# Performance work log

Measured on AMD Instinct MI355X. Metric: run time of the kernel, lower is better.

The kernel has to match this reference:

```python
import jax, jax.numpy as jnp
import numpy as np
import math

B, S, H = 2, 2048, 2048
NH, NKV, HD = 16, 4, 128


def _rope_tables(seq_len, head_dim):
    # Standard RoPE: freqs over half dim, duplicated to full head_dim.
    inv_freq = 1.0 / (10000.0 ** (np.arange(0, head_dim, 2, dtype=np.float32) / head_dim))
    t = np.arange(seq_len, dtype=np.float32)
    freqs = np.outer(t, inv_freq)  # [S, HD/2]
    emb = np.concatenate([freqs, freqs], axis=-1)  # [S, HD]
    return jnp.asarray(np.cos(emb)), jnp.asarray(np.sin(emb))


def setup_inputs() -> dict:
    key = jax.random.key(0)
    k1, k2, k3, k4 = jax.random.split(key, 4)
    cos, sin = _rope_tables(S, HD)
    return {
        "x": jax.random.normal(k1, (B, S, H), dtype=jnp.float32),
        "cos": cos,
        "sin": sin,
        "Wq": jax.random.normal(k2, (H, NH * HD), dtype=jnp.float32) * (1.0 / math.sqrt(H)),
        "Wkv": jax.random.normal(k3, (H, 2 * NKV * HD), dtype=jnp.float32) * (1.0 / math.sqrt(H)),
        "Wo": jax.random.normal(k4, (NH * HD, H), dtype=jnp.float32) * (1.0 / math.sqrt(NH * HD)),
    }


def _rotate_half(x):
    x1, x2 = jnp.split(x, 2, axis=-1)
    return jnp.concatenate([-x2, x1], axis=-1)


def _apply_rotary(x, cos, sin):
    # x: [B, S, nheads, HD]; cos/sin: [S, HD]
    c = cos[None, :, None, :]
    s = sin[None, :, None, :]
    return x * c + _rotate_half(x) * s


def reference(x, cos, sin, Wq, Wkv, Wo):
    b, s, _ = x.shape
    q = (x @ Wq).reshape(b, s, NH, HD)
    kv = x @ Wkv
    k, v = jnp.split(kv, [NKV * HD], axis=-1)
    k = k.reshape(b, s, NKV, HD)
    v = v.reshape(b, s, NKV, HD)
    q = _apply_rotary(q, cos, sin)
    k = _apply_rotary(k, cos, sin)
    # to [B, heads, S, HD]
    q = jnp.transpose(q, (0, 2, 1, 3))
    k = jnp.transpose(k, (0, 2, 1, 3))
    v = jnp.transpose(v, (0, 2, 1, 3))
    # GQA: repeat K/V heads
    rep = NH // NKV
    k = jnp.repeat(k, rep, axis=1)
    v = jnp.repeat(v, rep, axis=1)
    scale = jnp.asarray(1.0 / math.sqrt(HD), dtype=x.dtype)
    scores = jnp.einsum('bhqd,bhkd->bhqk', q * scale, k)  # [B, NH, S, S]
    causal = jnp.tril(jnp.ones((s, s), dtype=jnp.bool_))
    scores = jnp.where(causal, scores, jnp.asarray(-jnp.inf, scores.dtype))
    attn = jax.nn.softmax(scores, axis=-1)
    out = jnp.einsum('bhqk,bhkd->bhqd', attn, v)
    out = jnp.transpose(out, (0, 2, 1, 3)).reshape(b, s, NH * HD)
    return out @ Wo
```

## Files before the change

kernel.cpp:

```cpp
#include <hip/hip_runtime.h>
#include <math.h>

#define NB 2
#define SEQ 2048
#define HDIM 2048
#define NHD 16
#define NKVH 4
#define HEADD 128
#define MROWS (NB*SEQ)
#define NQCOLS (NHD*HEADD)
#define QKVCOLS 3072

typedef unsigned short ushortT;
typedef __attribute__((ext_vector_type(8))) short short8;
typedef __attribute__((ext_vector_type(4))) float floatx4;
typedef __attribute__((ext_vector_type(4))) unsigned short ushort4v;

__device__ __forceinline__ ushortT f2bf(float f) {
  union { float f; unsigned int u; } v; v.f = f;
  unsigned int r = v.u + 0x7FFFu + ((v.u >> 16) & 1u);
  return (ushortT)(r >> 16);
}
__device__ __forceinline__ float bf2f(ushortT u) {
  union { unsigned int u; float f; } v; v.u = ((unsigned int)u) << 16;
  return v.f;
}

__device__ __forceinline__ unsigned int cvt_pk_bf16(float lo, float hi) {
  unsigned int r;
  asm("v_cvt_pk_bf16_f32 %0, %1, %2" : "=v"(r) : "v"(lo), "v"(hi));
  return r;
}

__device__ __forceinline__ void gload16(const ushortT* g, ushortT* l) {
  __builtin_amdgcn_global_load_lds(
      (const __attribute__((address_space(1))) void*)g,
      (__attribute__((address_space(3))) void*)l, 16, 0, 0);
}

__device__ __forceinline__ void tile_barrier() {
  asm volatile("" ::: "memory");
  __builtin_amdgcn_s_barrier();
  asm volatile("" ::: "memory");
  __builtin_amdgcn_sched_barrier(0);
}

__global__ __launch_bounds__(256) void cast_bf16_kernel(
    const float* __restrict__ in, ushortT* __restrict__ out, int n4) {
  int i = blockIdx.x * 256 + threadIdx.x;
  if (i >= n4) return;
  float4 v = ((const float4*)in)[i];
  ushort4v o;
  o.x = f2bf(v.x); o.y = f2bf(v.y); o.z = f2bf(v.z); o.w = f2bf(v.w);
  ((ushort4v*)out)[i] = o;
}

__global__ __launch_bounds__(256) void transpose_cast3_kernel(
    const float* __restrict__ Wq, const float* __restrict__ Wkv,
    const float* __restrict__ Wo, ushortT* __restrict__ out) {
  __shared__ ushortT tile[32][33];
  int cu0 = blockIdx.x * 32, r0 = blockIdx.y * 32;
  const float* src; int C, c0;
  if (cu0 < 2048)      { src = Wq;  C = 2048; c0 = cu0; }
  else if (cu0 < 3072) { src = Wkv; C = 1024; c0 = cu0 - 2048; }
  else                 { src = Wo;  C = 2048; c0 = cu0 - 3072; }
  int tx = threadIdx.x & 31, ty = threadIdx.x >> 5;
#pragma unroll
  for (int i = 0; i < 4; ++i)
    tile[ty + i*8][tx] = f2bf(src[(size_t)(r0 + ty + i*8) * C + c0 + tx]);
  __syncthreads();
#pragma unroll
  for (int i = 0; i < 4; ++i)
    out[(size_t)(cu0 + ty + i*8) * 2048 + r0 + tx] = tile[tx][ty + i*8];
}

template <int MH>
__global__ __launch_bounds__(512, 2) void gemm_ring_kernel(
    const ushortT* __restrict__ A, const ushortT* __restrict__ Bt,
    void* __restrict__ C, int M, int N, int K, int c_fp32) {
  constexpr int BM = 128 * MH;
  __shared__ __align__(16) ushortT lA[4][BM * 32];
  __shared__ __align__(16) ushortT lB[4][256 * 32];
  const int m0 = blockIdx.y * BM;
  const int n0 = blockIdx.x * 256;
  const int tid = threadIdx.x;
  const int lane = tid & 63, wave = tid >> 6;
  const int g = lane >> 4, l15 = lane & 15;
  const int wr = wave >> 2, wc = wave & 3;
  const int wm = wr * (BM / 2), wn = wc * 64;

  floatx4 acc[4 * MH][4] = {};

  auto stageA = [&](int u) {
    ushortT* dst = lA[u & 3];
    const int kt = u << 5;
#pragma unroll
    for (int i = 0; i < MH; ++i) {
      int s = i * 512 + tid;
      int r = s >> 2, j = s & 3;
      int jj = j ^ ((r >> 1) & 3);
      gload16(A + (size_t)(m0 + r) * K + kt + jj * 8, dst + s * 8);
    }
  };
  auto stageB = [&](int u) {
    ushortT* dst = lB[u & 3];
    const int kt = u << 5;
#pragma unroll
    for (int i = 0; i < 2; ++i) {
      int s = i * 512 + tid;
      int r = s >> 2, j = s & 3;
      int jj = j ^ ((r >> 1) & 3);
      gload16(Bt + (size_t)(n0 + r) * K + kt + jj * 8, dst + s * 8);
    }
  };

  stageA(0); stageB(0); stageA(1); stageB(1); stageA(2); stageB(2);

  const int NT = K >> 5;
  for (int u = 0; u < NT; ++u) {
    if constexpr (MH == 2) {
      if (u + 2 < NT)      asm volatile("s_waitcnt vmcnt(8)" ::: "memory");
      else if (u + 1 < NT) asm volatile("s_waitcnt vmcnt(4)" ::: "memory");
      else                 asm volatile("s_waitcnt vmcnt(0)" ::: "memory");
    } else {
      if (u + 2 < NT)      asm volatile("s_waitcnt vmcnt(6)" ::: "memory");
      else if (u + 1 < NT) asm volatile("s_waitcnt vmcnt(3)" ::: "memory");
      else                 asm volatile("s_waitcnt vmcnt(0)" ::: "memory");
    }
    tile_barrier();

    const ushortT* la = lA[u & 3];
    const ushortT* lb = lB[u & 3];
    const bool more = (u + 3) < NT;

    short8 bfr[4];
#pragma unroll
    for (int nt = 0; nt < 4; ++nt) {
      int col = wn + nt * 16 + l15;
      bfr[nt] = *(const short8*)(lb + col * 32 + (g ^ ((col >> 1) & 3)) * 8);
    }

#pragma unroll
    for (int mh = 0; mh < MH; ++mh) {
      if (mh) tile_barrier();
      short8 afr[4];
#pragma unroll
      for (int mt = 0; mt < 4; ++mt) {
        int row = wm + mh * 64 + mt * 16 + l15;
        afr[mt] = *(const short8*)(la + row * 32 + (g ^ ((row >> 1) & 3)) * 8);
      }
      if (more) {
        if (mh == 0) stageA(u + 3);
        if (mh == MH - 1) stageB(u + 3);
      }
      __builtin_amdgcn_s_setprio(1);
#pragma unroll
      for (int mt = 0; mt < 4; ++mt)
#pragma unroll
        for (int nt = 0; nt < 4; ++nt)
          acc[mh * 4 + mt][nt] = __builtin_amdgcn_mfma_f32_16x16x32_bf16(
              afr[mt], bfr[nt], acc[mh * 4 + mt][nt], 0, 0, 0);
      __builtin_amdgcn_s_setprio(0);
    }
  }

#pragma unroll
  for (int fm = 0; fm < 4 * MH; ++fm)
#pragma unroll
    for (int nt = 0; nt < 4; ++nt)
#pragma unroll
      for (int r4 = 0; r4 < 4; ++r4) {
        int row = m0 + wm + fm * 16 + g * 4 + r4;
        int col = n0 + wn + nt * 16 + l15;
        float v = acc[fm][nt][r4];
        if (c_fp32) ((float*)C)[(size_t)row * N + col] = v;
        else ((ushortT*)C)[(size_t)row * N + col] = f2bf(v);
      }
}

__global__ __launch_bounds__(256) void rope_qk_kernel(
    const ushortT* __restrict__ QKVtmp, const float* __restrict__ cosT,
    const float* __restrict__ sinT, ushortT* __restrict__ Qr,
    ushortT* __restrict__ Kr) {
  int idx = blockIdx.x * 256 + threadIdx.x;
  if (idx < NB * SEQ * NHD * 64) {
    int d = idx & 63;
    int t = idx >> 6;
    int h = t & (NHD - 1);
    int bs = t >> 4;
    int s = bs & (SEQ - 1);
    int b = bs >> 11;
    float c = cosT[s * HEADD + d], sn = sinT[s * HEADD + d];
    float q1 = bf2f(QKVtmp[(size_t)bs * QKVCOLS + h * HEADD + d]);
    float q2 = bf2f(QKVtmp[(size_t)bs * QKVCOLS + h * HEADD + d + 64]);
    size_t o = ((size_t)(b * NHD + h) * SEQ + s) * HEADD + d;
    Qr[o]      = f2bf(q1 * c - q2 * sn);
    Qr[o + 64] = f2bf(q2 * c + q1 * sn);
  } else {
    int k = idx - NB * SEQ * NHD * 64;
    int d = k & 63;
    int t = k >> 6;
    int kvh = t & (NKVH - 1);
    int bs = t >> 2;
    int s = bs & (SEQ - 1);
    int b = bs >> 11;
    float c = cosT[s * HEADD + d], sn = sinT[s * HEADD + d];
    float k1 = bf2f(QKVtmp[(size_t)bs * QKVCOLS + 2048 + kvh * HEADD + d]);
    float k2 = bf2f(QKVtmp[(size_t)bs * QKVCOLS + 2048 + kvh * HEADD + d + 64]);
    size_t o = ((size_t)(b * NKVH + kvh) * SEQ + s) * HEADD + d;
    Kr[o]      = f2bf(k1 * c - k2 * sn);
    Kr[o + 64] = f2bf(k2 * c + k1 * sn);
  }
}

__global__ __launch_bounds__(256) void v_relayout_kernel(
    const ushortT* __restrict__ QKVtmp, ushortT* __restrict__ Vt) {
  __shared__ ushortT tile[32][33];
  int bk = blockIdx.z;
  int b = bk >> 2, kvh = bk & 3;
  int s0 = blockIdx.x * 32, d0 = blockIdx.y * 32;
  int tx = threadIdx.x & 31, ty = threadIdx.x >> 5;
#pragma unroll
  for (int i = 0; i < 4; ++i) {
    int s = s0 + ty + i * 8;
    tile[ty + i * 8][tx] =
        QKVtmp[(size_t)(b * SEQ + s) * QKVCOLS + 2560 + kvh * HEADD + d0 + tx];
  }
  __syncthreads();
#pragma unroll
  for (int i = 0; i < 4; ++i) {
    int d = d0 + ty + i * 8;
    Vt[((size_t)bk * HEADD + d) * SEQ + s0 + tx] = tile[tx][ty + i * 8];
  }
}

__global__ __launch_bounds__(256, 2) void attn_kernel(
    const ushortT* __restrict__ Q,
    const ushortT* __restrict__ Kg,
    const ushortT* __restrict__ Vg,
    ushortT* __restrict__ Oa) {
  __shared__ __align__(16) ushortT lK[2][64 * 128];
  __shared__ __align__(16) ushortT lV[2][128 * 64];
  __shared__ __align__(16) ushortT lP[4 * 32 * 64];

  const int tid = threadIdx.x;
  const int w = tid >> 6, lane = tid & 63;
  const int g = lane >> 4, l15 = lane & 15;
  const int sw = l15 & 7;
  const int bh = blockIdx.x;
  const int b = bh >> 4, h = bh & 15;
  const int kvh = h >> 2;
  const int yi = blockIdx.y;
  const int qi = (yi < 8) ? (15 - yi) : (yi - 8);
  const int q0 = qi << 7;
  const int qw = q0 + w * 32;
  const int nkt = 2 * qi + 2;

  const float SC = 0.08838834764831845f * 1.4426950408889634f;
  const float THR = 8.0f / SC;

  const ushortT* kbase = Kg + ((size_t)(b * NKVH + kvh)) * SEQ * HEADD;
  const ushortT* vbase = Vg + ((size_t)(b * NKVH + kvh)) * HEADD * SEQ;
  ushortT* pw = lP + w * 32 * 64;

  short8 qf[2][4];
#pragma unroll
  for (int mt = 0; mt < 2; ++mt) {
    const ushortT* qp =
        Q + (((size_t)(b * NHD + h)) * SEQ + qw + mt * 16 + l15) * HEADD + g * 8;
#pragma unroll
    for (int ks = 0; ks < 4; ++ks) qf[mt][ks] = *(const short8*)(qp + ks * 32);
  }

  floatx4 o[2][8] = {};
  float m_s[2] = {-INFINITY, -INFINITY};
  float l_s[2] = {0.f, 0.f};

  auto stage = [&](int kt, int buf) {
#pragma unroll
    for (int ii = 0; ii < 4; ++ii) {
      int s = ii * 256 + tid;
      int r = s >> 4, j = (s & 15) ^ (r & 7);
      gload16(kbase + (size_t)(kt * 64 + r) * HEADD + j * 8, lK[buf] + s * 8);
    }
#pragma unroll
    for (int ii = 0; ii < 4; ++ii) {
      int s = ii * 256 + tid;
      int r = s >> 3, j = (s & 7) ^ (r & 7);
      gload16(vbase + (size_t)r * SEQ + kt * 64 + j * 8, lV[buf] + s * 8);
    }
  };

  stage(0, 0);
  asm volatile("s_waitcnt vmcnt(0)" ::: "memory");
  __builtin_amdgcn_s_barrier();

  for (int kt = 0; kt < nkt; ++kt) {
    const int cur = kt & 1;
    if (kt + 1 < nkt) stage(kt + 1, cur ^ 1);

    const int kb = kt * 64;
    const int rel0 = qw - kb;
    const int rel1 = qw + 16 - kb;

    floatx4 sc[2][4] = {};
    __builtin_amdgcn_s_setprio(1);
#pragma unroll
    for (int nt = 0; nt < 4; ++nt) {
      if (nt * 16 > rel1 + 15) continue;
      const bool need0 = (nt * 16 <= rel0 + 15);
#pragma unroll
      for (int ks = 0; ks < 4; ++ks) {
        short8 kf = *(const short8*)(lK[cur] + (nt * 16 + l15) * 128 + ((ks * 4 + g) ^ sw) * 8);
        sc[1][nt] = __builtin_amdgcn_mfma_f32_16x16x32_bf16(kf, qf[1][ks], sc[1][nt], 0, 0, 0);
        if (need0)
          sc[0][nt] = __builtin_amdgcn_mfma_f32_16x16x32_bf16(kf, qf[0][ks], sc[0][nt], 0, 0, 0);
      }
    }
    __builtin_amdgcn_s_setprio(0);

#pragma unroll
    for (int mt = 0; mt < 2; ++mt) {
      const int qsub = qw + mt * 16;
      if (kb > qsub + 15) continue;
      const bool needmask = (kb + 63) > qsub;
      float ps[4][4];
      float mx = -INFINITY;
#pragma unroll
      for (int nt = 0; nt < 4; ++nt)
#pragma unroll
        for (int r = 0; r < 4; ++r) {
          float v = sc[mt][nt][r];
          if (needmask) {
            int kg = kb + nt * 16 + g * 4 + r;
            if (kg > qsub + l15) v = -INFINITY;
          }
          ps[nt][r] = v;
          mx = fmaxf(mx, v);
        }
      mx = fmaxf(mx, __shfl_xor(mx, 16));
      mx = fmaxf(mx, __shfl_xor(mx, 32));

      float mn;
      if (__all(mx <= m_s[mt] + THR)) {
        mn = m_s[mt];
      } else {
        mn = fmaxf(m_s[mt], mx);
        float alpha = __builtin_amdgcn_exp2f((m_s[mt] - mn) * SC);
        l_s[mt] *= alpha;
#pragma unroll
        for (int dt = 0; dt < 8; ++dt)
#pragma unroll
          for (int r = 0; r < 4; ++r) o[mt][dt][r] *= alpha;
        m_s[mt] = mn;
      }
      const float mnSC = mn * SC;

      float rs = 0.f;
#pragma unroll
      for (int nt = 0; nt < 4; ++nt) {
        float e[4];
#pragma unroll
        for (int r = 0; r < 4; ++r) {
          e[r] = __builtin_amdgcn_exp2f(__builtin_fmaf(ps[nt][r], SC, -mnSC));
          rs += e[r];
        }
        uint2 pk;
        pk.x = cvt_pk_bf16(e[0], e[1]);
        pk.y = cvt_pk_bf16(e[2], e[3]);
        *(uint2*)(pw + (mt * 16 + l15) * 64 +
                  (((nt * 2 + (g >> 1)) ^ sw) * 8 + (g & 1) * 4)) = pk;
      }
      rs += __shfl_xor(rs, 16);
      rs += __shfl_xor(rs, 32);
      l_s[mt] += rs;
    }

    __builtin_amdgcn_s_setprio(1);
#pragma unroll
    for (int ks = 0; ks < 2; ++ks) {
      const bool n1 = (kb + ks * 32 <= qw + 31);
      if (!n1) continue;
      const bool n0 = (kb + ks * 32 <= qw + 15);
      short8 bp1 = *(const short8*)(pw + (16 + l15) * 64 + ((ks * 4 + g) ^ sw) * 8);
      short8 bp0;
      if (n0) bp0 = *(const short8*)(pw + l15 * 64 + ((ks * 4 + g) ^ sw) * 8);
#pragma unroll
      for (int dt = 0; dt < 8; ++dt) {
        short8 vf = *(const short8*)(lV[cur] + (dt * 16 + l15) * 64 + ((ks * 4 + g) ^ sw) * 8);
        o[1][dt] = __builtin_amdgcn_mfma_f32_16x16x32_bf16(vf, bp1, o[1][dt], 0, 0, 0);
        if (n0)
          o[0][dt] = __builtin_amdgcn_mfma_f32_16x16x32_bf16(vf, bp0, o[0][dt], 0, 0, 0);
      }
    }
    __builtin_amdgcn_s_setprio(0);

    asm volatile("s_waitcnt vmcnt(0)" ::: "memory");
    __builtin_amdgcn_s_barrier();
  }

#pragma unroll
  for (int mt = 0; mt < 2; ++mt) {
    float inv = 1.f / l_s[mt];
    int qg = qw + mt * 16 + l15;
#pragma unroll
    for (int dt = 0; dt < 8; ++dt) {
      uint2 ov;
      ov.x = cvt_pk_bf16(o[mt][dt][0] * inv, o[mt][dt][1] * inv);
      ov.y = cvt_pk_bf16(o[mt][dt][2] * inv, o[mt][dt][3] * inv);
      *(uint2*)(Oa + (size_t)(b * SEQ + qg) * NQCOLS + h * HEADD + dt * 16 + g * 4) = ov;
    }
  }
}

extern "C" void kernel_launch(void* const* d_in, const int* in_sizes, int n_in,
                              void* d_out, int out_size, void* d_ws, size_t ws_size,
                              hipStream_t stream) {
  const float* x    = (const float*)d_in[0];
  const float* cosT = (const float*)d_in[1];
  const float* sinT = (const float*)d_in[2];
  const float* Wq   = (const float*)d_in[3];
  const float* Wkv  = (const float*)d_in[4];
  const float* Wo   = (const float*)d_in[5];

  char* ws = (char*)d_ws;
  ushortT* x_bf   = (ushortT*)(ws + 0);
  ushortT* Wqkvt  = (ushortT*)(ws + 16777216);
  ushortT* Wot    = (ushortT*)(ws + 29360128);
  ushortT* QKVtmp = (ushortT*)(ws + 37748736);
  ushortT* Qr     = (ushortT*)(ws + 62914560);
  ushortT* Kr     = (ushortT*)(ws + 79691776);
  ushortT* Vt     = (ushortT*)(ws + 83886080);
  ushortT* Oattn  = QKVtmp;

  cast_bf16_kernel<<<8192, 256, 0, stream>>>(x, x_bf, (MROWS * HDIM) / 4);
  transpose_cast3_kernel<<<dim3(160, 64), 256, 0, stream>>>(Wq, Wkv, Wo, Wqkvt);

  gemm_ring_kernel<2><<<dim3(12, 16), 512, 0, stream>>>(x_bf, Wqkvt, QKVtmp,
                                                        MROWS, QKVCOLS, HDIM, 0);

  rope_qk_kernel<<<20480, 256, 0, stream>>>(QKVtmp, cosT, sinT, Qr, Kr);
  v_relayout_kernel<<<dim3(64, 4, 8), 256, 0, stream>>>(QKVtmp, Vt);

  attn_kernel<<<dim3(32, 16), 256, 0, stream>>>(Qr, Kr, Vt, Oattn);

  gemm_ring_kernel<1><<<dim3(8, 32), 512, 0, stream>>>(Oattn, Wot, d_out,
                                                       MROWS, HDIM, NQCOLS, 1);
}
```

Measured before the change: 344.0 us.

## Pair causal query tiles per block with triple-buffered K/V pipeline

Each attention block now processes two query tiles (a long one and its short complement), so every block does the same amount of causal work, and the grid is halved. The K/V staging moves from double to triple buffering with partial vmcnt waits, letting loads run two tiles ahead and continue across the boundary between the two query tiles. Occupancy drops to one block per CU and LDS use rises, so latency hiding now relies on the deeper pipeline rather than a second resident block.

```diff
diff --git a/kernel.cpp b/kernel.cpp
--- a/kernel.cpp
+++ b/kernel.cpp
@@ -234,13 +234,13 @@
   }
 }
 
-__global__ __launch_bounds__(256, 2) void attn_kernel(
+__global__ __launch_bounds__(256, 1) void attn_kernel(
     const ushortT* __restrict__ Q,
     const ushortT* __restrict__ Kg,
     const ushortT* __restrict__ Vg,
     ushortT* __restrict__ Oa) {
-  __shared__ __align__(16) ushortT lK[2][64 * 128];
-  __shared__ __align__(16) ushortT lV[2][128 * 64];
+  __shared__ __align__(16) ushortT lK[3][64 * 128];
+  __shared__ __align__(16) ushortT lV[3][128 * 64];
   __shared__ __align__(16) ushortT lP[4 * 32 * 64];
 
   const int tid = threadIdx.x;
@@ -251,10 +251,10 @@
   const int b = bh >> 4, h = bh & 15;
   const int kvh = h >> 2;
   const int yi = blockIdx.y;
-  const int qi = (yi < 8) ? (15 - yi) : (yi - 8);
-  const int q0 = qi << 7;
-  const int qw = q0 + w * 32;
-  const int nkt = 2 * qi + 2;
+  const int qiA = 15 - yi;
+  const int qiB = yi;
+  const int nA = 2 * qiA + 2, nB = 2 * qiB + 2;
+  const int ntot = nA + nB;
 
   const float SC = 0.08838834764831845f * 1.4426950408889634f;
   const float THR = 8.0f / SC;
@@ -263,13 +263,21 @@
   const ushortT* vbase = Vg + ((size_t)(b * NKVH + kvh)) * HEADD * SEQ;
   ushortT* pw = lP + w * 32 * 64;
 
-  short8 qf[2][4];
+  const int qwA = (qiA << 7) + w * 32;
+  const int qwB = (qiB << 7) + w * 32;
+
+  short8 qfA[2][4], qfB[2][4];
 #pragma unroll
   for (int mt = 0; mt < 2; ++mt) {
-    const ushortT* qp =
-        Q + (((size_t)(b * NHD + h)) * SEQ + qw + mt * 16 + l15) * HEADD + g * 8;
-#pragma unroll
-    for (int ks = 0; ks < 4; ++ks) qf[mt][ks] = *(const short8*)(qp + ks * 32);
+    const ushortT* qpA =
+        Q + (((size_t)(b * NHD + h)) * SEQ + qwA + mt * 16 + l15) * HEADD + g * 8;
+    const ushortT* qpB =
+        Q + (((size_t)(b * NHD + h)) * SEQ + qwB + mt * 16 + l15) * HEADD + g * 8;
+#pragma unroll
+    for (int ks = 0; ks < 4; ++ks) {
+      qfA[mt][ks] = *(const short8*)(qpA + ks * 32);
+      qfB[mt][ks] = *(const short8*)(qpB + ks * 32);
+    }
   }
 
   floatx4 o[2][8] = {};
@@ -290,15 +298,11 @@
       gload16(vbase + (size_t)r * SEQ + kt * 64 + j * 8, lV[buf] + s * 8);
     }
   };
-
-  stage(0, 0);
-  asm volatile("s_waitcnt vmcnt(0)" ::: "memory");
-  __builtin_amdgcn_s_barrier();
-
-  for (int kt = 0; kt < nkt; ++kt) {
-    const int cur = kt & 1;
-    if (kt + 1 < nkt) stage(kt + 1, cur ^ 1);
-
+  auto stage_job = [&](int jj) {
+    if (jj < ntot) stage(jj < nA ? jj : jj - nA, jj % 3);
+  };
+
+  auto compute = [&](const short8 (&qf)[2][4], int qw, int kt, int cur) {
     const int kb = kt * 64;
     const int rel0 = qw - kb;
     const int rel1 = qw + 16 - kb;
@@ -394,23 +398,49 @@
       }
     }
     __builtin_amdgcn_s_setprio(0);
-
-    asm volatile("s_waitcnt vmcnt(0)" ::: "memory");
-    __builtin_amdgcn_s_barrier();
-  }
-
+  };
+
+  auto epilogue = [&](int qw) {
+#pragma unroll
+    for (int mt = 0; mt < 2; ++mt) {
+      float inv = 1.f / l_s[mt];
+      int qg = qw + mt * 16 + l15;
+#pragma unroll
+      for (int dt = 0; dt < 8; ++dt) {
+        uint2 ov;
+        ov.x = cvt_pk_bf16(o[mt][dt][0] * inv, o[mt][dt][1] * inv);
+        ov.y = cvt_pk_bf16(o[mt][dt][2] * inv, o[mt][dt][3] * inv);
+        *(uint2*)(Oa + (size_t)(b * SEQ + qg) * NQCOLS + h * HEADD + dt * 16 + g * 4) = ov;
+      }
+    }
+  };
+
+  stage_job(0);
+  stage_job(1);
+
+  for (int kt = 0; kt < nA; ++kt) {
+    asm volatile("s_waitcnt vmcnt(8)" ::: "memory");
+    tile_barrier();
+    stage_job(kt + 2);
+    compute(qfA, qwA, kt, kt % 3);
+  }
+  epilogue(qwA);
 #pragma unroll
   for (int mt = 0; mt < 2; ++mt) {
-    float inv = 1.f / l_s[mt];
-    int qg = qw + mt * 16 + l15;
-#pragma unroll
-    for (int dt = 0; dt < 8; ++dt) {
-      uint2 ov;
-      ov.x = cvt_pk_bf16(o[mt][dt][0] * inv, o[mt][dt][1] * inv);
-      ov.y = cvt_pk_bf16(o[mt][dt][2] * inv, o[mt][dt][3] * inv);
-      *(uint2*)(Oa + (size_t)(b * SEQ + qg) * NQCOLS + h * HEADD + dt * 16 + g * 4) = ov;
-    }
-  }
+#pragma unroll
+    for (int dt = 0; dt < 8; ++dt) o[mt][dt] = floatx4{0.f, 0.f, 0.f, 0.f};
+    m_s[mt] = -INFINITY; l_s[mt] = 0.f;
+  }
+
+  for (int kt = 0; kt < nB; ++kt) {
+    const int j = nA + kt;
+    if (j + 1 < ntot) asm volatile("s_waitcnt vmcnt(8)" ::: "memory");
+    else              asm volatile("s_waitcnt vmcnt(0)" ::: "memory");
+    tile_barrier();
+    stage_job(j + 2);
+    compute(qfB, qwB, kt, j % 3);
+  }
+  epilogue(qwB);
 }
 
 extern "C" void kernel_launch(void* const* d_in, const int* in_sizes, int n_in,
@@ -442,7 +472,7 @@
   rope_qk_kernel<<<20480, 256, 0, stream>>>(QKVtmp, cosT, sinT, Qr, Kr);
   v_relayout_kernel<<<dim3(64, 4, 8), 256, 0, stream>>>(QKVtmp, Vt);
 
-  attn_kernel<<<dim3(32, 16), 256, 0, stream>>>(Qr, Kr, Vt, Oattn);
+  attn_kernel<<<dim3(32, 8), 256, 0, stream>>>(Qr, Kr, Vt, Oattn);
 
   gemm_ring_kernel<1><<<dim3(8, 32), 512, 0, stream>>>(Oattn, Wot, d_out,
                                                        MROWS, HDIM, NQCOLS, 1);
```

Measured after the change: 360.0 us. +4.7%, slower.
